# Optimization experiments

Hardware: AMD Instinct MI355X
Metric: run time of the kernel (lower is better)

The kernel has to match this reference:

```python
import jax, jax.numpy as jnp
import numpy as np
import math

N = 50000
E = 800000
H = 128
AVG_DEGREE = 16


def setup_inputs() -> dict:
    key = jax.random.key(0)
    ks = jax.random.split(key, 6)
    x = jax.random.normal(ks[0], (N, H), dtype=jnp.float32)
    edge_index = jax.random.randint(ks[1], (2, E), 0, N, dtype=jnp.int64)
    # Kaiming-uniform-ish init like nn.Linear defaults (scale only matters for realism)
    W_interact = jax.random.normal(ks[2], (2 * H, H), dtype=jnp.float32) / np.sqrt(2 * H)
    b_interact = jnp.zeros((H,), dtype=jnp.float32)
    W_update = jax.random.normal(ks[3], (H, H), dtype=jnp.float32) / np.sqrt(H)
    b_update = jnp.zeros((H,), dtype=jnp.float32)
    return {
        "x": x,
        "edge_index": edge_index,
        "W_interact": W_interact,
        "b_interact": b_interact,
        "W_update": W_update,
        "b_update": b_update,
    }


def reference(x, edge_index, W_interact, b_interact, W_update, b_update):
    src, dst = edge_index[0], edge_index[1]
    # Edge gather + concat: [E, 2H]
    h_edge = jnp.concatenate([x[src], x[dst]], axis=-1)
    # interact linear + act -> messages m_ij: [E, H]
    m_ij = jax.nn.relu(h_edge @ W_interact + b_interact)
    # scatter-sum back to source nodes, normalized by sqrt(avg_degree)
    m_i = jax.ops.segment_sum(m_ij, src, num_segments=x.shape[0])
    m_i = m_i / jnp.asarray(math.sqrt(AVG_DEGREE), dtype=x.dtype)
    # residual update
    out = x + jax.nn.relu((x + m_i) @ W_update + b_update)
    return out
```

## Files before the change

kernel.cpp:

```cpp
#include <hip/hip_runtime.h>
#include <hip/hip_bf16.h>

#define H 128
#define NNODES 50000
#define NEDGES 800000
#define NBUK 1564
#define PAB 196
#define GEMMB 782
#define PRB 194
#define EB_CAP 768

using f32x4  = __attribute__((ext_vector_type(4))) float;
using bfrag8 = __attribute__((ext_vector_type(8))) short;

static __device__ __forceinline__ float bf2f(short s) {
    unsigned int u = ((unsigned int)(unsigned short)s) << 16;
    return __builtin_bit_cast(float, u);
}
static __device__ __forceinline__ short f2bf(float f) {
    unsigned int u = __builtin_bit_cast(unsigned int, f);
    unsigned int lsb = (u >> 16) & 1u;
    u += 0x7fffu + lsb;
    return (short)(u >> 16);
}

__global__ __launch_bounds__(256) void init_kernel(
    const unsigned int* __restrict__ xw, const int* __restrict__ ei,
    int* __restrict__ bcur, int* __restrict__ flags)
{
    const int gid = blockIdx.x * 256 + threadIdx.x;
    if (gid < NBUK) bcur[gid] = 0;
    if (blockIdx.x == 0 && threadIdx.x < 64) {
        int lane = threadIdx.x;
        unsigned int w = xw[lane];
        unsigned int e = (w >> 23) & 0xFFu;
        bool okf32 = (e >= 0x70u && e <= 0x8Fu);
        unsigned long long mf = __ballot(okf32);
        bool zero_odd = (ei[2 * lane + 1] == 0);
        unsigned long long mz = __ballot(zero_odd);
        if (lane == 0) {
            flags[0] = (__popcll(mf) > 32) ? 1 : 0;
            flags[1] = (mz == ~0ULL) ? 1 : 0;
        }
    }
}

__global__ __launch_bounds__(256) void prep_kernel(
    const void* __restrict__ Wi, const void* __restrict__ Wu,
    const void* __restrict__ bi, const void* __restrict__ bu,
    short* __restrict__ WtPQ, short* __restrict__ WtU,
    float* __restrict__ bI, float* __restrict__ bU,
    const int* __restrict__ flags)
{
    const bool isf = flags[0] != 0;
    int i = blockIdx.x * 256 + threadIdx.x;
    if (i < 256 * 128) {
        int c = i >> 7, k = i & 127;
        int srcidx = (c < 128) ? (k * 128 + c) : ((128 + k) * 128 + (c - 128));
        short v = isf ? f2bf(((const float*)Wi)[srcidx]) : ((const short*)Wi)[srcidx];
        WtPQ[c * 128 + k] = v;
    } else if (i < 32768 + 128 * 128) {
        int j = i - 32768;
        int k = j >> 7, n = j & 127;
        short v = isf ? f2bf(((const float*)Wu)[j]) : ((const short*)Wu)[j];
        WtU[n * 128 + k] = v;
    } else if (i < 49152 + 128) {
        int j = i - 49152;
        bI[j] = isf ? ((const float*)bi)[j] : bf2f(((const short*)bi)[j]);
    } else if (i < 49152 + 256) {
        int j = i - 49152 - 128;
        bU[j] = isf ? ((const float*)bu)[j] : bf2f(((const short*)bu)[j]);
    }
}

__global__ __launch_bounds__(256) void gemm_bin_kernel(
    const void* __restrict__ xin, const short* __restrict__ WtPQ,
    const float* __restrict__ bI, short* __restrict__ PQb,
    const int* __restrict__ ei, int* __restrict__ bcur,
    unsigned int* __restrict__ ebuf, const int* __restrict__ flags)
{
    const int t = threadIdx.x;
    const bool isf = flags[0] != 0;

    if (blockIdx.x < PAB) {
        __shared__ int cnt[NBUK], lcur[NBUK], gbase[NBUK];
        for (int j = t; j < NBUK; j += 256) { cnt[j] = 0; lcur[j] = 0; }
        __syncthreads();
        const bool e64 = flags[1] != 0;
        const int base = blockIdx.x * 4096;
        int sv[16], dv[16];
        #pragma unroll
        for (int k = 0; k < 16; ++k) {
            int e = base + k * 256 + t;
            if (e < NEDGES) {
                if (e64) {
                    sv[k] = (int)((const long long*)ei)[e];
                    dv[k] = (int)((const long long*)ei)[NEDGES + e];
                } else {
                    sv[k] = ei[e];
                    dv[k] = ei[NEDGES + e];
                }
                atomicAdd(&cnt[sv[k] >> 5], 1);
            } else sv[k] = -1;
        }
        __syncthreads();
        for (int j = t; j < NBUK; j += 256)
            if (cnt[j] > 0) gbase[j] = atomicAdd(&bcur[j], cnt[j]);
        __syncthreads();
        #pragma unroll
        for (int k = 0; k < 16; ++k) {
            if (sv[k] >= 0) {
                int b = sv[k] >> 5;
                int l = atomicAdd(&lcur[b], 1);
                int slot = gbase[b] + l;
                if (slot < EB_CAP)
                    ebuf[b * EB_CAP + slot] =
                        ((unsigned int)(sv[k] & 31) << 16) | (unsigned int)dv[k];
            }
        }
    } else {
        __shared__ short sA[64][136];
        const int row0 = (blockIdx.x - PAB) * 64;

        #pragma unroll
        for (int it = 0; it < 4; ++it) {
            int idx = it * 256 + t;
            int row = idx >> 4, ch = idx & 15;
            int grow = row0 + row; if (grow >= NNODES) grow = NNODES - 1;
            if (isf) {
                const float* xf = (const float*)xin + (size_t)grow * H + ch * 8;
                f32x4 a = *reinterpret_cast<const f32x4*>(xf);
                f32x4 b = *reinterpret_cast<const f32x4*>(xf + 4);
                short o[8];
                #pragma unroll
                for (int j = 0; j < 4; ++j) { o[j] = f2bf(a[j]); o[4 + j] = f2bf(b[j]); }
                *reinterpret_cast<uint4*>(&sA[row][ch * 8]) = *reinterpret_cast<uint4*>(o);
            } else {
                *reinterpret_cast<uint4*>(&sA[row][ch * 8]) =
                    *reinterpret_cast<const uint4*>((const short*)xin + (size_t)grow * H + ch * 8);
            }
        }
        __syncthreads();

        const int lane = t & 63;
        const int w    = t >> 6;
        const int r0   = (w >> 1) * 32;
        const int c0   = (w & 1) * 128;
        const int lr   = lane & 15;
        const int lk   = (lane >> 4) * 8;

        f32x4 acc[2][8];
        #pragma unroll
        for (int m = 0; m < 2; ++m)
            #pragma unroll
            for (int n = 0; n < 8; ++n) acc[m][n] = (f32x4){0.f, 0.f, 0.f, 0.f};

        #pragma unroll
        for (int k0 = 0; k0 < 4; ++k0) {
            int k = k0 * 32 + lk;
            bfrag8 a0 = *reinterpret_cast<const bfrag8*>(&sA[r0 + lr][k]);
            bfrag8 a1 = *reinterpret_cast<const bfrag8*>(&sA[r0 + 16 + lr][k]);
            #pragma unroll
            for (int n = 0; n < 8; ++n) {
                bfrag8 b = *reinterpret_cast<const bfrag8*>(&WtPQ[(c0 + n * 16 + lr) * 128 + k]);
                acc[0][n] = __builtin_amdgcn_mfma_f32_16x16x32_bf16(a0, b, acc[0][n], 0, 0, 0);
                acc[1][n] = __builtin_amdgcn_mfma_f32_16x16x32_bf16(a1, b, acc[1][n], 0, 0, 0);
            }
        }

        float bias[8];
        #pragma unroll
        for (int n = 0; n < 8; ++n) {
            int col = c0 + n * 16 + lr;
            bias[n] = (col < 128) ? bI[col] : 0.f;
        }

        const int rbase = (lane >> 4) * 4;
        #pragma unroll
        for (int m = 0; m < 2; ++m) {
            #pragma unroll
            for (int r = 0; r < 4; ++r) {
                int grow = row0 + r0 + m * 16 + rbase + r;
                if (grow < NNODES) {
                    #pragma unroll
                    for (int n = 0; n < 8; ++n) {
                        int col = c0 + n * 16 + lr;
                        PQb[grow * 256 + col] = f2bf(acc[m][n][r] + bias[n]);
                    }
                }
            }
        }
    }
}

__global__ __launch_bounds__(256) void fused_out_kernel(
    const void* __restrict__ xin, const short* __restrict__ PQb,
    const unsigned int* __restrict__ ebuf, const int* __restrict__ bcur,
    const short* __restrict__ WtU, const float* __restrict__ bU,
    float* __restrict__ out, const int* __restrict__ flags)
{
    __shared__ short sA[32][136];
    __shared__ unsigned int es[EB_CAP];
    __shared__ unsigned short ds_[EB_CAP];
    __shared__ int cnt_s[32];
    __shared__ int loff[33];

    const int t = threadIdx.x, b = blockIdx.x;
    const int node0 = b * 32;
    const bool isf = flags[0] != 0;

    int ne = bcur[b]; if (ne > EB_CAP) ne = EB_CAP;
    const int e0 = b * EB_CAP;

    if (t < 32) cnt_s[t] = 0;
    __syncthreads();

    for (int e = t; e < ne; e += 256) {
        unsigned int v = ebuf[e0 + e];
        es[e] = v;
        atomicAdd(&cnt_s[v >> 16], 1);
    }
    __syncthreads();

    if (t < 32) {
        int c = cnt_s[t];
        int val = c;
        #pragma unroll
        for (int off = 1; off < 32; off <<= 1) {
            int up = __shfl_up(val, off);
            if (t >= off) val += up;
        }
        int excl = val - c;
        loff[t]  = excl;
        cnt_s[t] = excl;
        if (t == 31) loff[32] = val;
    }
    __syncthreads();

    for (int e = t; e < ne; e += 256) {
        unsigned int v = es[e];
        int slot = atomicAdd(&cnt_s[v >> 16], 1);
        ds_[slot] = (unsigned short)(v & 0xFFFFu);
    }
    __syncthreads();

    const int lane = t & 63, w = t >> 6;
    const int c2 = lane * 2;
    for (int j8 = 0; j8 < 8; ++j8) {
        const int j = w * 8 + j8;
        const int i = node0 + j;
        if (i >= NNODES) {
            *reinterpret_cast<unsigned int*>(&sA[j][c2]) = 0;
            continue;
        }
        unsigned int pw = *reinterpret_cast<const unsigned int*>(PQb + i * 256 + c2);
        float p0 = bf2f((short)(pw & 0xFFFF)), p1 = bf2f((short)(pw >> 16));
        float a0 = 0.f, a1 = 0.f;
        const int lo = loff[j], hi = loff[j + 1];
        int e = lo;
        for (; e + 8 <= hi; e += 8) {
            unsigned int q[8];
            #pragma unroll
            for (int jj = 0; jj < 8; ++jj) {
                int dn = ds_[e + jj];
                q[jj] = *reinterpret_cast<const unsigned int*>(PQb + dn * 256 + 128 + c2);
            }
            #pragma unroll
            for (int jj = 0; jj < 8; ++jj) {
                float s0 = p0 + bf2f((short)(q[jj] & 0xFFFF));
                float s1 = p1 + bf2f((short)(q[jj] >> 16));
                a0 += (s0 > 0.f) ? s0 : 0.f;
                a1 += (s1 > 0.f) ? s1 : 0.f;
            }
        }
        for (; e < hi; ++e) {
            int dn = ds_[e];
            unsigned int qw = *reinterpret_cast<const unsigned int*>(PQb + dn * 256 + 128 + c2);
            float s0 = p0 + bf2f((short)(qw & 0xFFFF));
            float s1 = p1 + bf2f((short)(qw >> 16));
            a0 += (s0 > 0.f) ? s0 : 0.f;
            a1 += (s1 > 0.f) ? s1 : 0.f;
        }
        float x0, x1;
        if (isf) {
            const float* xf = (const float*)xin + (size_t)i * H + c2;
            x0 = xf[0]; x1 = xf[1];
        } else {
            unsigned int xw = *reinterpret_cast<const unsigned int*>(
                (const short*)xin + (size_t)i * H + c2);
            x0 = bf2f((short)(xw & 0xFFFF)); x1 = bf2f((short)(xw >> 16));
        }
        short r0 = f2bf(x0 + 0.25f * a0), r1 = f2bf(x1 + 0.25f * a1);
        *reinterpret_cast<unsigned int*>(&sA[j][c2]) =
            (unsigned int)(unsigned short)r0 | ((unsigned int)(unsigned short)r1 << 16);
    }
    __syncthreads();

    const int c0g = w * 32;
    const int lr  = lane & 15;
    const int lk  = (lane >> 4) * 8;

    f32x4 acc[2][2];
    #pragma unroll
    for (int m = 0; m < 2; ++m)
        #pragma unroll
        for (int n = 0; n < 2; ++n) acc[m][n] = (f32x4){0.f, 0.f, 0.f, 0.f};

    #pragma unroll
    for (int k0 = 0; k0 < 4; ++k0) {
        int k = k0 * 32 + lk;
        bfrag8 a0 = *reinterpret_cast<const bfrag8*>(&sA[lr][k]);
        bfrag8 a1 = *reinterpret_cast<const bfrag8*>(&sA[16 + lr][k]);
        #pragma unroll
        for (int n = 0; n < 2; ++n) {
            bfrag8 bb = *reinterpret_cast<const bfrag8*>(&WtU[(c0g + n * 16 + lr) * 128 + k]);
            acc[0][n] = __builtin_amdgcn_mfma_f32_16x16x32_bf16(a0, bb, acc[0][n], 0, 0, 0);
            acc[1][n] = __builtin_amdgcn_mfma_f32_16x16x32_bf16(a1, bb, acc[1][n], 0, 0, 0);
        }
    }

    float bias[2];
    #pragma unroll
    for (int n = 0; n < 2; ++n) bias[n] = bU[c0g + n * 16 + lr];

    const int rbase = (lane >> 4) * 4;
    #pragma unroll
    for (int m = 0; m < 2; ++m) {
        #pragma unroll
        for (int r = 0; r < 4; ++r) {
            int grow = node0 + m * 16 + rbase + r;
            if (grow < NNODES) {
                #pragma unroll
                for (int n = 0; n < 2; ++n) {
                    int col = c0g + n * 16 + lr;
                    float v = acc[m][n][r] + bias[n];
                    v = v > 0.f ? v : 0.f;
                    float xv = isf ? ((const float*)xin)[(size_t)grow * H + col]
                                   : bf2f(((const short*)xin)[(size_t)grow * H + col]);
                    out[(size_t)grow * H + col] = xv + v;
                }
            }
        }
    }
}

extern "C" void kernel_launch(void* const* d_in, const int* in_sizes, int n_in,
                              void* d_out, int out_size, void* d_ws, size_t ws_size,
                              hipStream_t stream) {
    const void* x  = d_in[0];
    const int*  ei = (const int*)d_in[1];
    const void* Wi = d_in[2];
    const void* bi = d_in[3];
    const void* Wu = d_in[4];
    const void* bu = d_in[5];

    char* ws = (char*)d_ws;
    short*        PQb   = (short*)(ws);
    unsigned int* ebuf  = (unsigned int*)(ws + 25600000);
    int*          bcur  = (int*)  (ws + 30404608);
    short*        WtPQ  = (short*)(ws + 30411008);
    short*        WtU   = (short*)(ws + 30476544);
    float*        bI    = (float*)(ws + 30509312);
    float*        bU    = (float*)(ws + 30509824);
    int*          flags = (int*)  (ws + 30510336);

    init_kernel<<<7, 256, 0, stream>>>((const unsigned int*)x, ei, bcur, flags);
    prep_kernel<<<PRB, 256, 0, stream>>>(Wi, Wu, bi, bu, WtPQ, WtU, bI, bU, flags);
    gemm_bin_kernel<<<PAB + GEMMB, 256, 0, stream>>>(
        x, WtPQ, bI, PQb, ei, bcur, ebuf, flags);
    fused_out_kernel<<<NBUK, 256, 0, stream>>>(
        x, PQb, ebuf, bcur, WtU, bU, (float*)d_out, flags);
}
```

Before: 94.04 us.

## Store Q half in FP8 e4m3 and bin edges into 64-node buckets

Splits the PQ projection buffer into a bf16 P array and an FP8 (e4m3) Q array, halving the bytes read for each per-edge gathered Q row. Edge binning now uses 64-node buckets, and each pair of fused-output blocks rescans the shared bucket, filtering edges by half and reading ebuf from global twice instead of staging it in LDS. The FP8 quantization of Q reduces accuracy of messages and may exceed tolerance; the doubled ebuf scan adds some redundant reads.

Measured after the change: 117.7 us. 25.2% more time.

```diff
diff --git a/kernel.cpp b/kernel.cpp
--- a/kernel.cpp
+++ b/kernel.cpp
@@ -4,11 +4,12 @@
 #define H 128
 #define NNODES 50000
 #define NEDGES 800000
-#define NBUK 1564
+#define NBK_BIN 782
+#define NFB 1564
 #define PAB 196
 #define GEMMB 782
 #define PRB 194
-#define EB_CAP 768
+#define EB_CAP 1536
 
 using f32x4  = __attribute__((ext_vector_type(4))) float;
 using bfrag8 = __attribute__((ext_vector_type(8))) short;
@@ -23,13 +24,37 @@
     u += 0x7fffu + lsb;
     return (short)(u >> 16);
 }
+static __device__ __forceinline__ unsigned char f2e4m3(float f) {
+    unsigned int u = __builtin_bit_cast(unsigned int, f);
+    unsigned int s = (u >> 24) & 0x80u;
+    unsigned int au = u & 0x7FFFFFFFu;
+    float af = __builtin_bit_cast(float, au);
+    if (af >= 448.f) return (unsigned char)(s | 0x7Eu);
+    if (af < 0.015625f) {
+        int m = (int)rintf(af * 512.f);
+        return (unsigned char)(s | (unsigned int)m);
+    }
+    unsigned int lsb = (au >> 20) & 1u;
+    au += 0x7FFFFu + lsb;
+    unsigned int em = (au >> 20) - (120u << 3);
+    if (em > 0x7Eu) em = 0x7Eu;
+    return (unsigned char)(s | em);
+}
+static __device__ __forceinline__ float e4m3f(unsigned int c) {
+    unsigned int em = c & 0x7Fu;
+    unsigned int s  = (c & 0x80u) << 24;
+    float nrm = __builtin_bit_cast(float, s | ((em << 20) + 0x3C000000u));
+    float sub = (float)(int)em * 0.001953125f;
+    sub = (c & 0x80u) ? -sub : sub;
+    return (em >= 8u) ? nrm : sub;
+}
 
 __global__ __launch_bounds__(256) void init_kernel(
     const unsigned int* __restrict__ xw, const int* __restrict__ ei,
     int* __restrict__ bcur, int* __restrict__ flags)
 {
     const int gid = blockIdx.x * 256 + threadIdx.x;
-    if (gid < NBUK) bcur[gid] = 0;
+    if (gid < NBK_BIN) bcur[gid] = 0;
     if (blockIdx.x == 0 && threadIdx.x < 64) {
         int lane = threadIdx.x;
         unsigned int w = xw[lane];
@@ -75,7 +100,8 @@
 
 __global__ __launch_bounds__(256) void gemm_bin_kernel(
     const void* __restrict__ xin, const short* __restrict__ WtPQ,
-    const float* __restrict__ bI, short* __restrict__ PQb,
+    const float* __restrict__ bI, short* __restrict__ Pb,
+    unsigned char* __restrict__ Qb8,
     const int* __restrict__ ei, int* __restrict__ bcur,
     unsigned int* __restrict__ ebuf, const int* __restrict__ flags)
 {
@@ -83,8 +109,8 @@
     const bool isf = flags[0] != 0;
 
     if (blockIdx.x < PAB) {
-        __shared__ int cnt[NBUK], lcur[NBUK], gbase[NBUK];
-        for (int j = t; j < NBUK; j += 256) { cnt[j] = 0; lcur[j] = 0; }
+        __shared__ int cnt[NBK_BIN], lcur[NBK_BIN], gbase[NBK_BIN];
+        for (int j = t; j < NBK_BIN; j += 256) { cnt[j] = 0; lcur[j] = 0; }
         __syncthreads();
         const bool e64 = flags[1] != 0;
         const int base = blockIdx.x * 4096;
@@ -100,22 +126,22 @@
                     sv[k] = ei[e];
                     dv[k] = ei[NEDGES + e];
                 }
-                atomicAdd(&cnt[sv[k] >> 5], 1);
+                atomicAdd(&cnt[sv[k] >> 6], 1);
             } else sv[k] = -1;
         }
         __syncthreads();
-        for (int j = t; j < NBUK; j += 256)
+        for (int j = t; j < NBK_BIN; j += 256)
             if (cnt[j] > 0) gbase[j] = atomicAdd(&bcur[j], cnt[j]);
         __syncthreads();
         #pragma unroll
         for (int k = 0; k < 16; ++k) {
             if (sv[k] >= 0) {
-                int b = sv[k] >> 5;
+                int b = sv[k] >> 6;
                 int l = atomicAdd(&lcur[b], 1);
                 int slot = gbase[b] + l;
                 if (slot < EB_CAP)
                     ebuf[b * EB_CAP + slot] =
-                        ((unsigned int)(sv[k] & 31) << 16) | (unsigned int)dv[k];
+                        ((unsigned int)(sv[k] & 63) << 16) | (unsigned int)dv[k];
             }
         }
     } else {
@@ -168,57 +194,68 @@
             }
         }
 
-        float bias[8];
-        #pragma unroll
-        for (int n = 0; n < 8; ++n) {
-            int col = c0 + n * 16 + lr;
-            bias[n] = (col < 128) ? bI[col] : 0.f;
-        }
-
         const int rbase = (lane >> 4) * 4;
-        #pragma unroll
-        for (int m = 0; m < 2; ++m) {
-            #pragma unroll
-            for (int r = 0; r < 4; ++r) {
-                int grow = row0 + r0 + m * 16 + rbase + r;
-                if (grow < NNODES) {
-                    #pragma unroll
-                    for (int n = 0; n < 8; ++n) {
-                        int col = c0 + n * 16 + lr;
-                        PQb[grow * 256 + col] = f2bf(acc[m][n][r] + bias[n]);
+        if (c0 == 0) {
+            float bias[8];
+            #pragma unroll
+            for (int n = 0; n < 8; ++n) bias[n] = bI[n * 16 + lr];
+            #pragma unroll
+            for (int m = 0; m < 2; ++m) {
+                #pragma unroll
+                for (int r = 0; r < 4; ++r) {
+                    int grow = row0 + r0 + m * 16 + rbase + r;
+                    if (grow < NNODES) {
+                        #pragma unroll
+                        for (int n = 0; n < 8; ++n)
+                            Pb[(size_t)grow * H + n * 16 + lr] = f2bf(acc[m][n][r] + bias[n]);
                     }
                 }
             }
+        } else {
+            #pragma unroll
+            for (int m = 0; m < 2; ++m) {
+                #pragma unroll
+                for (int r = 0; r < 4; ++r) {
+                    int grow = row0 + r0 + m * 16 + rbase + r;
+                    if (grow < NNODES) {
+                        #pragma unroll
+                        for (int n = 0; n < 8; ++n)
+                            Qb8[(size_t)grow * H + n * 16 + lr] = f2e4m3(acc[m][n][r]);
+                    }
+                }
+            }
         }
     }
 }
 
 __global__ __launch_bounds__(256) void fused_out_kernel(
-    const void* __restrict__ xin, const short* __restrict__ PQb,
+    const void* __restrict__ xin, const short* __restrict__ Pb,
+    const unsigned char* __restrict__ Qb8,
     const unsigned int* __restrict__ ebuf, const int* __restrict__ bcur,
     const short* __restrict__ WtU, const float* __restrict__ bU,
     float* __restrict__ out, const int* __restrict__ flags)
 {
     __shared__ short sA[32][136];
-    __shared__ unsigned int es[EB_CAP];
-    __shared__ unsigned short ds_[EB_CAP];
+    __shared__ unsigned short ds_[EB_CAP / 2];
     __shared__ int cnt_s[32];
     __shared__ int loff[33];
 
     const int t = threadIdx.x, b = blockIdx.x;
+    const int cb = b >> 1;
+    const unsigned int half = (unsigned int)(b & 1);
     const int node0 = b * 32;
     const bool isf = flags[0] != 0;
 
-    int ne = bcur[b]; if (ne > EB_CAP) ne = EB_CAP;
-    const int e0 = b * EB_CAP;
+    int ne = bcur[cb]; if (ne > EB_CAP) ne = EB_CAP;
+    const unsigned int* __restrict__ ep = ebuf + (size_t)cb * EB_CAP;
 
     if (t < 32) cnt_s[t] = 0;
     __syncthreads();
 
     for (int e = t; e < ne; e += 256) {
-        unsigned int v = ebuf[e0 + e];
-        es[e] = v;
-        atomicAdd(&cnt_s[v >> 16], 1);
+        unsigned int v = ep[e];
+        unsigned int ls = v >> 16;
+        if ((ls >> 5) == half) atomicAdd(&cnt_s[ls & 31], 1);
     }
     __syncthreads();
 
@@ -238,9 +275,12 @@
     __syncthreads();
 
     for (int e = t; e < ne; e += 256) {
-        unsigned int v = es[e];
-        int slot = atomicAdd(&cnt_s[v >> 16], 1);
-        ds_[slot] = (unsigned short)(v & 0xFFFFu);
+        unsigned int v = ep[e];
+        unsigned int ls = v >> 16;
+        if ((ls >> 5) == half) {
+            int slot = atomicAdd(&cnt_s[ls & 31], 1);
+            ds_[slot] = (unsigned short)(v & 0xFFFFu);
+        }
     }
     __syncthreads();
 
@@ -253,7 +293,7 @@
             *reinterpret_cast<unsigned int*>(&sA[j][c2]) = 0;
             continue;
         }
-        unsigned int pw = *reinterpret_cast<const unsigned int*>(PQb + i * 256 + c2);
+        unsigned int pw = *reinterpret_cast<const unsigned int*>(Pb + (size_t)i * H + c2);
         float p0 = bf2f((short)(pw & 0xFFFF)), p1 = bf2f((short)(pw >> 16));
         float a0 = 0.f, a1 = 0.f;
         const int lo = loff[j], hi = loff[j + 1];
@@ -263,21 +303,21 @@
             #pragma unroll
             for (int jj = 0; jj < 8; ++jj) {
                 int dn = ds_[e + jj];
-                q[jj] = *reinterpret_cast<const unsigned int*>(PQb + dn * 256 + 128 + c2);
+                q[jj] = *reinterpret_cast<const unsigned short*>(Qb8 + (size_t)dn * H + c2);
             }
             #pragma unroll
             for (int jj = 0; jj < 8; ++jj) {
-                float s0 = p0 + bf2f((short)(q[jj] & 0xFFFF));
-                float s1 = p1 + bf2f((short)(q[jj] >> 16));
+                float s0 = p0 + e4m3f(q[jj] & 0xFFu);
+                float s1 = p1 + e4m3f(q[jj] >> 8);
                 a0 += (s0 > 0.f) ? s0 : 0.f;
                 a1 += (s1 > 0.f) ? s1 : 0.f;
             }
         }
         for (; e < hi; ++e) {
             int dn = ds_[e];
-            unsigned int qw = *reinterpret_cast<const unsigned int*>(PQb + dn * 256 + 128 + c2);
-            float s0 = p0 + bf2f((short)(qw & 0xFFFF));
-            float s1 = p1 + bf2f((short)(qw >> 16));
+            unsigned int qw = *reinterpret_cast<const unsigned short*>(Qb8 + (size_t)dn * H + c2);
+            float s0 = p0 + e4m3f(qw & 0xFFu);
+            float s1 = p1 + e4m3f(qw >> 8);
             a0 += (s0 > 0.f) ? s0 : 0.f;
             a1 += (s1 > 0.f) ? s1 : 0.f;
         }
@@ -355,19 +395,20 @@
     const void* bu = d_in[5];
 
     char* ws = (char*)d_ws;
-    short*        PQb   = (short*)(ws);
-    unsigned int* ebuf  = (unsigned int*)(ws + 25600000);
-    int*          bcur  = (int*)  (ws + 30404608);
-    short*        WtPQ  = (short*)(ws + 30411008);
-    short*        WtU   = (short*)(ws + 30476544);
-    float*        bI    = (float*)(ws + 30509312);
-    float*        bU    = (float*)(ws + 30509824);
-    int*          flags = (int*)  (ws + 30510336);
-
-    init_kernel<<<7, 256, 0, stream>>>((const unsigned int*)x, ei, bcur, flags);
+    short*         Pb    = (short*)(ws);
+    unsigned char* Qb8   = (unsigned char*)(ws + 12800000);
+    unsigned int*  ebuf  = (unsigned int*)(ws + 19200000);
+    int*           bcur  = (int*)  (ws + 24004608);
+    short*         WtPQ  = (short*)(ws + 24007808);
+    short*         WtU   = (short*)(ws + 24073344);
+    float*         bI    = (float*)(ws + 24106112);
+    float*         bU    = (float*)(ws + 24106624);
+    int*           flags = (int*)  (ws + 24107136);
+
+    init_kernel<<<4, 256, 0, stream>>>((const unsigned int*)x, ei, bcur, flags);
     prep_kernel<<<PRB, 256, 0, stream>>>(Wi, Wu, bi, bu, WtPQ, WtU, bI, bU, flags);
     gemm_bin_kernel<<<PAB + GEMMB, 256, 0, stream>>>(
-        x, WtPQ, bI, PQb, ei, bcur, ebuf, flags);
-    fused_out_kernel<<<NBUK, 256, 0, stream>>>(
-        x, PQb, ebuf, bcur, WtU, bU, (float*)d_out, flags);
-}
+        x, WtPQ, bI, Pb, Qb8, ei, bcur, ebuf, flags);
+    fused_out_kernel<<<NFB, 256, 0, stream>>>(
+        x, Pb, Qb8, ebuf, bcur, WtU, bU, (float*)d_out, flags);
+}
```
